# Kernel tuning notes

Measured on AMD Instinct MI355X. Metric: run time of the kernel, lower is better.

The kernel has to match this reference:

```python
import jax, jax.numpy as jnp
import numpy as np

B, S, IN, D, H, L, M = 8, 1024, 256, 512, 8, 2, 64
DK = D // H
FF = 4 * D
EPS = 1e-5


def setup_inputs() -> dict:
    key = jax.random.key(0)
    ks = jax.random.split(key, 16)
    w = lambda k, shape: jax.random.normal(k, shape, jnp.float32) * 0.02
    return {
        "inputs": jax.random.normal(ks[0], (B, S, IN), jnp.float32),
        "lengths": jax.random.randint(ks[1], (B,), S // 2, S + 1),
        "W_in": w(ks[2], (IN, D)), "b_in": jnp.zeros((D,), jnp.float32),
        # per-layer stacked params (leading axis L) for lax.scan
        "Wq": w(ks[3], (L, D, D)), "bq": jnp.zeros((L, D), jnp.float32),
        "Wk": w(ks[4], (L, D, D)), "bk": jnp.zeros((L, D), jnp.float32),
        "Wv": w(ks[5], (L, D, D)), "bv": jnp.zeros((L, D), jnp.float32),
        "Wo": w(ks[6], (L, D, D)), "bo": jnp.zeros((L, D), jnp.float32),
        "rel_bias": w(ks[7], (L, H, 2 * M - 1)),
        "W1": w(ks[8], (L, D, FF)), "b1": jnp.zeros((L, FF), jnp.float32),
        "W2": w(ks[9], (L, FF, D)), "b2": jnp.zeros((L, D), jnp.float32),
        "g1": jnp.ones((L, D), jnp.float32), "be1": jnp.zeros((L, D), jnp.float32),
        "g2": jnp.ones((L, D), jnp.float32), "be2": jnp.zeros((L, D), jnp.float32),
        "gf": jnp.ones((D,), jnp.float32), "bef": jnp.zeros((D,), jnp.float32),
    }


def _ln(x, g, b):
    m = jnp.mean(x, axis=-1, keepdims=True)
    v = jnp.mean(jnp.square(x - m), axis=-1, keepdims=True)
    return (x - m) * jax.lax.rsqrt(v + EPS) * g + b


def _sinusoid_pe(seq_len, d_model):
    pos = jnp.arange(seq_len, dtype=jnp.float32)[:, None]
    div = jnp.exp(jnp.arange(0, d_model, 2, dtype=jnp.float32) * (-np.log(10000.0) / d_model))
    pe = jnp.zeros((seq_len, d_model), jnp.float32)
    pe = pe.at[:, 0::2].set(jnp.sin(pos * div))
    pe = pe.at[:, 1::2].set(jnp.cos(pos * div))
    return pe


def _encoder(inputs, lengths, W_in, b_in, Wq, bq, Wk, bk, Wv, bv, Wo, bo,
             rel_bias, W1, b1, W2, b2, g1, be1, g2, be2, gf, bef):
    x = inputs @ W_in + b_in                      # (B,S,D)
    x = x + _sinusoid_pe(S, D)[None]
    pad = jnp.arange(S)[None, :] >= lengths[:, None]   # (B,S) True = padded key

    r = jnp.arange(S)
    rel_idx = jnp.clip(r[:, None] - r[None, :], -(M - 1), M - 1) + (M - 1)  # (S,S)
    scale = 1.0 / np.sqrt(DK)

    def layer(x, p):
        (wq, bq_, wk, bk_, wv, bv_, wo, bo_, rb, w1, b1_, w2, b2_, g1_, be1_, g2_, be2_) = p
        # --- self-attention sublayer (pre-norm) ---
        h = _ln(x, g1_, be1_)
        q = (h @ wq + bq_).reshape(B, S, H, DK).transpose(0, 2, 1, 3)  # (B,H,S,DK)
        k = (h @ wk + bk_).reshape(B, S, H, DK).transpose(0, 2, 1, 3)
        v = (h @ wv + bv_).reshape(B, S, H, DK).transpose(0, 2, 1, 3)
        scores = jnp.einsum('bhqd,bhkd->bhqk', q, k) * scale
        scores = scores + rb[:, rel_idx][None]            # (H,S,S) relative bias
        scores = jnp.where(pad[:, None, None, :], -jnp.inf, scores)
        attn = jax.nn.softmax(scores, axis=-1)
        o = jnp.einsum('bhqk,bhkd->bhqd', attn, v)
        o = o.transpose(0, 2, 1, 3).reshape(B, S, D) @ wo + bo_
        x = x + o
        # --- FFN sublayer (pre-norm) ---
        h = _ln(x, g2_, be2_)
        x = x + (jax.nn.relu(h @ w1 + b1_) @ w2 + b2_)
        return x, None

    stacked = (Wq, bq, Wk, bk, Wv, bv, Wo, bo, rel_bias, W1, b1, W2, b2, g1, be1, g2, be2)
    x, _ = jax.lax.scan(layer, x, stacked)
    return _ln(x, gf, bef)


def reference(inputs, lengths, W_in, b_in, Wq, bq, Wk, bk, Wv, bv, Wo, bo,
              rel_bias, W1, b1, W2, b2, g1, be1, g2, be2, gf, bef):
    return _encoder(inputs, lengths, W_in, b_in, Wq, bq, Wk, bk, Wv, bv, Wo, bo,
                    rel_bias, W1, b1, W2, b2, g1, be1, g2, be2, gf, bef)
```

## Files before the change

kernel.cpp:

```cpp
#include <hip/hip_runtime.h>
#include <hip/hip_bf16.h>

typedef unsigned short u16;
typedef unsigned int u32;
typedef __bf16 v8bf __attribute__((ext_vector_type(8)));
typedef float v4f __attribute__((ext_vector_type(4)));

#define B_SZ 8
#define S_LEN 1024
#define IN_DIM 256
#define DMODEL 512
#define NHEAD 8
#define DK 64
#define FF_DIM 2048
#define MROWS (B_SZ * S_LEN)
#define QSCALE 0.1803368801111204f

__device__ __forceinline__ u16 f2bf(float f) {
    unsigned int x = __float_as_uint(f);
    unsigned int r = (x + 0x7fffu + ((x >> 16) & 1u)) >> 16;
    return (u16)r;
}

__device__ __forceinline__ void gl16(const u16* g, u16* l) {
    __builtin_amdgcn_global_load_lds((const __attribute__((address_space(1))) unsigned int*)g,
                                     (__attribute__((address_space(3))) unsigned int*)l, 16, 0, 0);
}

__global__ __launch_bounds__(256) void conv_bf16_kernel(const float* __restrict__ in,
                                                        u16* __restrict__ out, int n4) {
    int i = blockIdx.x * 256 + threadIdx.x;
    if (i < n4) {
        float4 v = ((const float4*)in)[i];
        ushort4 o;
        o.x = f2bf(v.x); o.y = f2bf(v.y); o.z = f2bf(v.z); o.w = f2bf(v.w);
        ((ushort4*)out)[i] = o;
    }
}

struct TDesc { const float* src; u16* dst; int K; int N; };
struct TArgs { TDesc d[13]; };

__global__ void transpose_conv_kernel(TArgs args) {
    TDesc t = args.d[blockIdx.z];
    int k0 = blockIdx.x * 32, n0 = blockIdx.y * 32;
    if (k0 >= t.K || n0 >= t.N) return;
    __shared__ float tile[32][33];
    int tx = threadIdx.x, ty = threadIdx.y;
#pragma unroll
    for (int j = 0; j < 4; j++) {
        int k = k0 + ty + j * 8;
        tile[ty + j * 8][tx] = t.src[(size_t)k * t.N + n0 + tx];
    }
    __syncthreads();
#pragma unroll
    for (int j = 0; j < 4; j++) {
        int n = n0 + ty + j * 8;
        t.dst[(size_t)n * t.K + k0 + tx] = f2bf(tile[tx][ty + j * 8]);
    }
}

template <bool OUT_BF16>
__global__ __launch_bounds__(256) void ln_kernel(const float* __restrict__ x,
                                                 const float* __restrict__ g,
                                                 const float* __restrict__ b,
                                                 void* __restrict__ out) {
    int row = blockIdx.x * 4 + (threadIdx.x >> 6);
    int lane = threadIdx.x & 63;
    const float4* xr = (const float4*)(x + (size_t)row * DMODEL);
    float4 v0 = xr[lane], v1 = xr[lane + 64];
    float s = v0.x + v0.y + v0.z + v0.w + v1.x + v1.y + v1.z + v1.w;
    float sq = v0.x * v0.x + v0.y * v0.y + v0.z * v0.z + v0.w * v0.w +
               v1.x * v1.x + v1.y * v1.y + v1.z * v1.z + v1.w * v1.w;
#pragma unroll
    for (int m = 1; m < 64; m <<= 1) {
        s += __shfl_xor(s, m);
        sq += __shfl_xor(sq, m);
    }
    float mean = s * (1.0f / DMODEL);
    float var = sq * (1.0f / DMODEL) - mean * mean;
    float rstd = rsqrtf(var + 1e-5f);
    const float4* g4 = (const float4*)g;
    const float4* b4 = (const float4*)b;
    float4 ga = g4[lane], gb = g4[lane + 64], ba = b4[lane], bb = b4[lane + 64];
    float4 r0, r1;
    r0.x = (v0.x - mean) * rstd * ga.x + ba.x;
    r0.y = (v0.y - mean) * rstd * ga.y + ba.y;
    r0.z = (v0.z - mean) * rstd * ga.z + ba.z;
    r0.w = (v0.w - mean) * rstd * ga.w + ba.w;
    r1.x = (v1.x - mean) * rstd * gb.x + bb.x;
    r1.y = (v1.y - mean) * rstd * gb.y + bb.y;
    r1.z = (v1.z - mean) * rstd * gb.z + bb.z;
    r1.w = (v1.w - mean) * rstd * gb.w + bb.w;
    if (OUT_BF16) {
        ushort4 o0, o1;
        o0.x = f2bf(r0.x); o0.y = f2bf(r0.y); o0.z = f2bf(r0.z); o0.w = f2bf(r0.w);
        o1.x = f2bf(r1.x); o1.y = f2bf(r1.y); o1.z = f2bf(r1.z); o1.w = f2bf(r1.w);
        ((ushort4*)out)[(size_t)row * 128 + lane] = o0;
        ((ushort4*)out)[(size_t)row * 128 + 64 + lane] = o1;
    } else {
        ((float4*)out)[(size_t)row * 128 + lane] = r0;
        ((float4*)out)[(size_t)row * 128 + 64 + lane] = r1;
    }
}

template <int MT, int NT>
__device__ __forceinline__ void gemm_core(const u16* __restrict__ A, const u16* __restrict__ Bt,
                                          int K, v4f (&acc)[MT][NT]) {
    constexpr int BM = MT * 32;
    constexpr int BN = NT * 32;
    __shared__ u16 As[BM * 64];
    __shared__ u16 Bs[BN * 64];
    int tid = threadIdx.x;
    int n0 = blockIdx.x * BN, m0 = blockIdx.y * BM;
    int w = tid >> 6, lane = tid & 63;
    int wr = (w >> 1) * (BM / 2), wc = (w & 1) * (BN / 2);
    int lr = lane & 15, lq = lane >> 4;
    int r8 = lane >> 3, cb = lane & 7;
    int scol = (cb ^ r8) * 8;

    v4f zero = {0.f, 0.f, 0.f, 0.f};
#pragma unroll
    for (int i = 0; i < MT; i++)
#pragma unroll
        for (int j = 0; j < NT; j++) acc[i][j] = zero;

    const u16* gA[MT]; u16* lA[MT];
#pragma unroll
    for (int j = 0; j < MT; j++) {
        int row0 = (MT * 8) * w + j * 8;
        gA[j] = A + (size_t)(m0 + row0 + r8) * K + scol;
        lA[j] = As + row0 * 64;
    }
    const u16* gB[NT]; u16* lB[NT];
#pragma unroll
    for (int j = 0; j < NT; j++) {
        int row0 = (NT * 8) * w + j * 8;
        gB[j] = Bt + (size_t)(n0 + row0 + r8) * K + scol;
        lB[j] = Bs + row0 * 64;
    }

    for (int k0 = 0; k0 < K; k0 += 64) {
#pragma unroll
        for (int j = 0; j < MT; j++) gl16(gA[j], lA[j]);
#pragma unroll
        for (int j = 0; j < NT; j++) gl16(gB[j], lB[j]);
        __syncthreads();
#pragma unroll
        for (int kk = 0; kk < 2; kk++) {
            int xb = ((kk * 4 + lq) ^ (lr & 7)) * 8;
            v8bf af[MT], bfr[NT];
#pragma unroll
            for (int i = 0; i < MT; i++)
                af[i] = *(const v8bf*)&As[(wr + i * 16 + lr) * 64 + xb];
#pragma unroll
            for (int j = 0; j < NT; j++)
                bfr[j] = *(const v8bf*)&Bs[(wc + j * 16 + lr) * 64 + xb];
#pragma unroll
            for (int mt = 0; mt < MT; mt++)
#pragma unroll
                for (int nt = 0; nt < NT; nt++)
                    acc[mt][nt] = __builtin_amdgcn_mfma_f32_16x16x32_bf16(af[mt], bfr[nt], acc[mt][nt], 0, 0, 0);
        }
        __syncthreads();
#pragma unroll
        for (int j = 0; j < MT; j++) gA[j] += 64;
#pragma unroll
        for (int j = 0; j < NT; j++) gB[j] += 64;
    }
}

__global__ __launch_bounds__(256) void gemm_in_kernel(const u16* __restrict__ A,
                                                      const u16* __restrict__ Bt,
                                                      const float* __restrict__ bias,
                                                      float* __restrict__ Out, int K) {
    v4f acc[4][2];
    gemm_core<4, 2>(A, Bt, K, acc);
    int tid = threadIdx.x, w = tid >> 6, lane = tid & 63;
    int lr = lane & 15, lq = lane >> 4;
    int wr = (w >> 1) * 64, wc = (w & 1) * 32;
    int n0 = blockIdx.x * 64, m0 = blockIdx.y * 128;
#pragma unroll
    for (int mt = 0; mt < 4; mt++) {
#pragma unroll
        for (int nt = 0; nt < 2; nt++) {
            int col = n0 + wc + nt * 16 + lr;
            float bcol = bias[col];
            float freq = __builtin_amdgcn_exp2f((float)(col & ~1) * (-0.025953277f));
#pragma unroll
            for (int reg = 0; reg < 4; reg++) {
                int row = m0 + wr + mt * 16 + lq * 4 + reg;
                float rev = (float)(row & (S_LEN - 1)) * freq * 0.15915494309189535f;
                float fr = __builtin_amdgcn_fractf(rev);
                float pe = (col & 1) ? __builtin_amdgcn_cosf(fr) : __builtin_amdgcn_sinf(fr);
                Out[(size_t)row * DMODEL + col] = acc[mt][nt][reg] + bcol + pe;
            }
        }
    }
}

__global__ __launch_bounds__(256) void gemm_qkv_kernel(const u16* __restrict__ A,
                                                       const u16* __restrict__ Bt,
                                                       const float* __restrict__ bq,
                                                       const float* __restrict__ bk,
                                                       const float* __restrict__ bv,
                                                       u16* __restrict__ Qo,
                                                       u16* __restrict__ Ko,
                                                       u16* __restrict__ Vto, int K) {
    v4f acc[4][4];
    gemm_core<4, 4>(A, Bt, K, acc);
    int tid = threadIdx.x, w = tid >> 6, lane = tid & 63;
    int lr = lane & 15, lq = lane >> 4;
    int wr = (w >> 1) * 64, wc = (w & 1) * 64;
    int n0 = blockIdx.x * 128, m0 = blockIdx.y * 128;
    int seg = n0 >> 9;
#pragma unroll
    for (int mt = 0; mt < 4; mt++) {
#pragma unroll
        for (int nt = 0; nt < 4; nt++) {
            int col = (n0 + wc + nt * 16 + lr) & (DMODEL - 1);
            if (seg == 0) {
                float bcol = bq[col];
#pragma unroll
                for (int reg = 0; reg < 4; reg++) {
                    int row = m0 + wr + mt * 16 + lq * 4 + reg;
                    Qo[(size_t)row * DMODEL + col] = f2bf((acc[mt][nt][reg] + bcol) * QSCALE);
                }
            } else if (seg == 1) {
                float bcol = bk[col];
#pragma unroll
                for (int reg = 0; reg < 4; reg++) {
                    int row = m0 + wr + mt * 16 + lq * 4 + reg;
                    Ko[(size_t)row * DMODEL + col] = f2bf(acc[mt][nt][reg] + bcol);
                }
            } else {
                float bcol = bv[col];
                int row0 = m0 + wr + mt * 16 + lq * 4;
                int bb = row0 >> 10, s0 = row0 & (S_LEN - 1);
                ushort4 o;
                o.x = f2bf(acc[mt][nt][0] + bcol);
                o.y = f2bf(acc[mt][nt][1] + bcol);
                o.z = f2bf(acc[mt][nt][2] + bcol);
                o.w = f2bf(acc[mt][nt][3] + bcol);
                *(ushort4*)(Vto + ((size_t)(bb * DMODEL + col)) * S_LEN + s0) = o;
            }
        }
    }
}

__global__ __launch_bounds__(256) void gemm_relu_kernel(const u16* __restrict__ A,
                                                        const u16* __restrict__ Bt,
                                                        const float* __restrict__ bias,
                                                        u16* __restrict__ Out, int N, int K) {
    v4f acc[4][4];
    gemm_core<4, 4>(A, Bt, K, acc);
    int tid = threadIdx.x, w = tid >> 6, lane = tid & 63;
    int lr = lane & 15, lq = lane >> 4;
    int wr = (w >> 1) * 64, wc = (w & 1) * 64;
    int n0 = blockIdx.x * 128, m0 = blockIdx.y * 128;
#pragma unroll
    for (int mt = 0; mt < 4; mt++) {
#pragma unroll
        for (int nt = 0; nt < 4; nt++) {
            int col = n0 + wc + nt * 16 + lr;
            float bcol = bias[col];
#pragma unroll
            for (int reg = 0; reg < 4; reg++) {
                int row = m0 + wr + mt * 16 + lq * 4 + reg;
                Out[(size_t)row * N + col] = f2bf(fmaxf(acc[mt][nt][reg] + bcol, 0.0f));
            }
        }
    }
}

__global__ __launch_bounds__(256) void gemm_res_kernel(const u16* __restrict__ A,
                                                       const u16* __restrict__ Bt,
                                                       const float* __restrict__ bias,
                                                       float* __restrict__ Out, int K) {
    v4f acc[4][2];
    gemm_core<4, 2>(A, Bt, K, acc);
    int tid = threadIdx.x, w = tid >> 6, lane = tid & 63;
    int lr = lane & 15, lq = lane >> 4;
    int wr = (w >> 1) * 64, wc = (w & 1) * 32;
    int n0 = blockIdx.x * 64, m0 = blockIdx.y * 128;
#pragma unroll
    for (int mt = 0; mt < 4; mt++) {
#pragma unroll
        for (int nt = 0; nt < 2; nt++) {
            int col = n0 + wc + nt * 16 + lr;
            float bcol = bias[col];
#pragma unroll
            for (int reg = 0; reg < 4; reg++) {
                int row = m0 + wr + mt * 16 + lq * 4 + reg;
                size_t idx = (size_t)row * DMODEL + col;
                Out[idx] = Out[idx] + acc[mt][nt][reg] + bcol;
            }
        }
    }
}

#define LDP 68
__global__ __launch_bounds__(256) void fattn_kernel(const u16* __restrict__ Qg,
                                                    const u16* __restrict__ Kg,
                                                    const u16* __restrict__ Vtg,
                                                    const float* __restrict__ rb,
                                                    const int* __restrict__ lengths,
                                                    u16* __restrict__ O) {
    int qt = blockIdx.x, h = blockIdx.y, b = blockIdx.z;
    int tid = threadIdx.x, w = tid >> 6, lane = tid & 63;
    int lr = lane & 15, lq = lane >> 4;
    __shared__ u16 Ks[2][64 * 64];
    __shared__ u16 Vs[2][64 * 64];
    __shared__ u16 Pw[4][32 * LDP];
    __shared__ float rbs[128];
    int len = lengths[b];
    if (tid < 127) rbs[tid] = rb[h * 127 + tid] * 1.4426950408889634f;

    int qw = qt * 128 + w * 32;
    v8bf qa[2][2];
#pragma unroll
    for (int ntq = 0; ntq < 2; ntq++) {
        size_t qrow = ((size_t)(b * S_LEN + qw + ntq * 16 + lr)) * DMODEL + h * DK;
        qa[ntq][0] = *(const v8bf*)(Qg + qrow + lq * 8);
        qa[ntq][1] = *(const v8bf*)(Qg + qrow + 32 + lq * 8);
    }

    v4f zero = {0.f, 0.f, 0.f, 0.f};
    v4f Oacc[2][4];
#pragma unroll
    for (int mt = 0; mt < 2; mt++)
#pragma unroll
        for (int nt = 0; nt < 4; nt++) Oacc[mt][nt] = zero;
    float lsum[2] = {0.f, 0.f};

    const u16* Kbase = Kg + ((size_t)b * S_LEN) * DMODEL + h * DK;
    const u16* Vbase = Vtg + ((size_t)(b * DMODEL + h * DK)) * S_LEN;
    u16* P = Pw[w];
    int r8 = lane >> 3, cb = lane & 7;
    int swz = (cb ^ r8) * 8;

#pragma unroll
    for (int j = 0; j < 2; j++) {
        int row0 = w * 16 + j * 8;
        gl16(Kbase + (size_t)(row0 + r8) * DMODEL + swz, Ks[0] + row0 * 64);
        gl16(Vbase + (size_t)(row0 + r8) * S_LEN + swz, Vs[0] + row0 * 64);
    }

    int pb = 0;
    for (int kb0 = 0; kb0 < len; kb0 += 64, pb ^= 1) {
        __syncthreads();
        __builtin_amdgcn_sched_barrier(0);

        int nxt = kb0 + 64;
        if (nxt < len) {
#pragma unroll
            for (int j = 0; j < 2; j++) {
                int row0 = w * 16 + j * 8;
                gl16(Kbase + (size_t)(nxt + row0 + r8) * DMODEL + swz, Ks[pb ^ 1] + row0 * 64);
                gl16(Vbase + (size_t)(row0 + r8) * S_LEN + nxt + swz, Vs[pb ^ 1] + row0 * 64);
            }
        }
        const u16* Ksc = Ks[pb];
        const u16* Vsc = Vs[pb];

        v8bf kf[4][2];
#pragma unroll
        for (int mtk = 0; mtk < 4; mtk++) {
#pragma unroll
            for (int half = 0; half < 2; half++) {
                int xb = ((half * 4 + lq) ^ (lr & 7)) * 8;
                kf[mtk][half] = *(const v8bf*)&Ksc[(mtk * 16 + lr) * 64 + xb];
            }
        }

        v4f S[4][2];
#pragma unroll
        for (int mtk = 0; mtk < 4; mtk++)
#pragma unroll
            for (int ntq = 0; ntq < 2; ntq++) {
                v4f s = __builtin_amdgcn_mfma_f32_16x16x32_bf16(kf[mtk][0], qa[ntq][0], zero, 0, 0, 0);
                S[mtk][ntq] = __builtin_amdgcn_mfma_f32_16x16x32_bf16(kf[mtk][1], qa[ntq][1], s, 0, 0, 0);
            }

        bool edge = (kb0 + 64 > len);
        int dmin = qw - (kb0 + 63), dmax = qw + 31 - kb0;
        bool perel = !(dmax <= -63 || dmin >= 63);
        float bconst = (dmax <= -63) ? rbs[0] : rbs[126];
#pragma unroll
        for (int mtk = 0; mtk < 4; mtk++) {
#pragma unroll
            for (int ntq = 0; ntq < 2; ntq++) {
                int q = qw + ntq * 16 + lr;
                float p[4];
#pragma unroll
                for (int r = 0; r < 4; r++) {
                    int key = kb0 + mtk * 16 + lq * 4 + r;
                    float s = S[mtk][ntq][r];
                    if (perel) {
                        int d = q - key;
                        d = d < -63 ? -63 : (d > 63 ? 63 : d);
                        s += rbs[d + 63];
                    } else {
                        s += bconst;
                    }
                    float pv = __builtin_amdgcn_exp2f(s);
                    if (edge && key >= len) pv = 0.f;
                    lsum[ntq] += pv;
                    p[r] = pv;
                }
                uint2 pk;
                pk.x = (__float_as_uint(p[1]) & 0xffff0000u) | (__float_as_uint(p[0]) >> 16);
                pk.y = (__float_as_uint(p[3]) & 0xffff0000u) | (__float_as_uint(p[2]) >> 16);
                *(uint2*)&P[(ntq * 16 + lr) * LDP + mtk * 16 + lq * 4] = pk;
            }
        }

        v8bf vb[4][2];
#pragma unroll
        for (int ntd = 0; ntd < 4; ntd++) {
#pragma unroll
            for (int half = 0; half < 2; half++) {
                int xb = ((half * 4 + lq) ^ (lr & 7)) * 8;
                vb[ntd][half] = *(const v8bf*)&Vsc[(ntd * 16 + lr) * 64 + xb];
            }
        }
#pragma unroll
        for (int mtq = 0; mtq < 2; mtq++) {
            v8bf pa0 = *(const v8bf*)&P[(mtq * 16 + lr) * LDP + lq * 8];
            v8bf pa1 = *(const v8bf*)&P[(mtq * 16 + lr) * LDP + 32 + lq * 8];
#pragma unroll
            for (int ntd = 0; ntd < 4; ntd++) {
                Oacc[mtq][ntd] = __builtin_amdgcn_mfma_f32_16x16x32_bf16(pa0, vb[ntd][0], Oacc[mtq][ntd], 0, 0, 0);
                Oacc[mtq][ntd] = __builtin_amdgcn_mfma_f32_16x16x32_bf16(pa1, vb[ntd][1], Oacc[mtq][ntd], 0, 0, 0);
            }
        }
    }

    float lsumR[2];
#pragma unroll
    for (int ntq = 0; ntq < 2; ntq++) {
        float s = lsum[ntq];
        s += __shfl_xor(s, 16);
        s += __shfl_xor(s, 32);
        lsumR[ntq] = s;
    }
#pragma unroll
    for (int mtq = 0; mtq < 2; mtq++) {
        float inv[4];
#pragma unroll
        for (int r = 0; r < 4; r++)
            inv[r] = 1.0f / __shfl(lsumR[mtq], lq * 4 + r);
        size_t obase = ((size_t)(b * S_LEN + qw + mtq * 16)) * DMODEL + h * DK;
#pragma unroll
        for (int ntd = 0; ntd < 4; ntd++)
#pragma unroll
            for (int r = 0; r < 4; r++)
                O[obase + (size_t)(lq * 4 + r) * DMODEL + ntd * 16 + lr] = f2bf(Oacc[mtq][ntd][r] * inv[r]);
    }
}

extern "C" void kernel_launch(void* const* d_in, const int* in_sizes, int n_in,
                              void* d_out, int out_size, void* d_ws, size_t ws_size,
                              hipStream_t stream) {
    const float* inputs   = (const float*)d_in[0];
    const int*   lengths  = (const int*)d_in[1];
    const float* W_in     = (const float*)d_in[2];
    const float* b_in     = (const float*)d_in[3];
    const float* Wq       = (const float*)d_in[4];
    const float* bq       = (const float*)d_in[5];
    const float* Wk       = (const float*)d_in[6];
    const float* bk       = (const float*)d_in[7];
    const float* Wv       = (const float*)d_in[8];
    const float* bv       = (const float*)d_in[9];
    const float* Wo       = (const float*)d_in[10];
    const float* bo       = (const float*)d_in[11];
    const float* rel_bias = (const float*)d_in[12];
    const float* W1       = (const float*)d_in[13];
    const float* b1       = (const float*)d_in[14];
    const float* W2       = (const float*)d_in[15];
    const float* b2       = (const float*)d_in[16];
    const float* g1       = (const float*)d_in[17];
    const float* be1      = (const float*)d_in[18];
    const float* g2       = (const float*)d_in[19];
    const float* be2      = (const float*)d_in[20];
    const float* gf       = (const float*)d_in[21];
    const float* bef      = (const float*)d_in[22];

    char* ws = (char*)d_ws;
    float* xbuf = (float*)ws;          ws += (size_t)MROWS * DMODEL * 4;
    u16* hbuf   = (u16*)ws;            ws += (size_t)MROWS * DMODEL * 2;
    u16* aobuf  = hbuf;
    u16* qbf    = (u16*)ws;            ws += (size_t)MROWS * FF_DIM * 2;
    u16* kbf    = qbf + (size_t)MROWS * DMODEL;
    u16* vtbf   = kbf + (size_t)MROWS * DMODEL;
    u16* tbuf   = qbf;
    u16* inbf   = qbf;
    u16* wt_in  = (u16*)ws;            ws += (size_t)DMODEL * IN_DIM * 2;
    u16 *qkvw[2], *wto[2], *wt1[2], *wt2[2];
    for (int l = 0; l < 2; l++) { qkvw[l] = (u16*)ws; ws += (size_t)3 * DMODEL * DMODEL * 2; }
    for (int l = 0; l < 2; l++) { wto[l] = (u16*)ws; ws += (size_t)DMODEL * DMODEL * 2; }
    for (int l = 0; l < 2; l++) { wt1[l] = (u16*)ws; ws += (size_t)FF_DIM * DMODEL * 2; }
    for (int l = 0; l < 2; l++) { wt2[l] = (u16*)ws; ws += (size_t)DMODEL * FF_DIM * 2; }

    TArgs ta;
    int ti = 0;
    ta.d[ti++] = {W_in, wt_in, IN_DIM, DMODEL};
    for (int l = 0; l < 2; l++) {
        ta.d[ti++] = {Wq + (size_t)l * DMODEL * DMODEL, qkvw[l], DMODEL, DMODEL};
        ta.d[ti++] = {Wk + (size_t)l * DMODEL * DMODEL, qkvw[l] + (size_t)DMODEL * DMODEL, DMODEL, DMODEL};
        ta.d[ti++] = {Wv + (size_t)l * DMODEL * DMODEL, qkvw[l] + (size_t)2 * DMODEL * DMODEL, DMODEL, DMODEL};
        ta.d[ti++] = {Wo + (size_t)l * DMODEL * DMODEL, wto[l], DMODEL, DMODEL};
        ta.d[ti++] = {W1 + (size_t)l * DMODEL * FF_DIM, wt1[l], DMODEL, FF_DIM};
        ta.d[ti++] = {W2 + (size_t)l * FF_DIM * DMODEL, wt2[l], FF_DIM, DMODEL};
    }

    conv_bf16_kernel<<<dim3((MROWS * IN_DIM / 4 + 255) / 256), 256, 0, stream>>>(
        inputs, inbf, MROWS * IN_DIM / 4);
    transpose_conv_kernel<<<dim3(64, 64, 13), dim3(32, 8), 0, stream>>>(ta);

    gemm_in_kernel<<<dim3(DMODEL / 64, MROWS / 128), 256, 0, stream>>>(
        inbf, wt_in, b_in, xbuf, IN_DIM);

    for (int l = 0; l < 2; l++) {
        ln_kernel<true><<<MROWS / 4, 256, 0, stream>>>(xbuf, g1 + l * DMODEL, be1 + l * DMODEL, hbuf);
        gemm_qkv_kernel<<<dim3(3 * DMODEL / 128, MROWS / 128), 256, 0, stream>>>(
            hbuf, qkvw[l], bq + l * DMODEL, bk + l * DMODEL, bv + l * DMODEL,
            qbf, kbf, vtbf, DMODEL);
        fattn_kernel<<<dim3(S_LEN / 128, NHEAD, B_SZ), 256, 0, stream>>>(
            qbf, kbf, vtbf, rel_bias + (size_t)l * NHEAD * 127, lengths, aobuf);
        gemm_res_kernel<<<dim3(DMODEL / 64, MROWS / 128), 256, 0, stream>>>(
            aobuf, wto[l], bo + l * DMODEL, xbuf, DMODEL);
        ln_kernel<true><<<MROWS / 4, 256, 0, stream>>>(xbuf, g2 + l * DMODEL, be2 + l * DMODEL, hbuf);
        gemm_relu_kernel<<<dim3(FF_DIM / 128, MROWS / 128), 256, 0, stream>>>(
            hbuf, wt1[l], b1 + l * FF_DIM, tbuf, FF_DIM, DMODEL);
        gemm_res_kernel<<<dim3(DMODEL / 64, MROWS / 128), 256, 0, stream>>>(
            tbuf, wt2[l], b2 + l * DMODEL, xbuf, FF_DIM);
    }
    ln_kernel<false><<<MROWS / 4, 256, 0, stream>>>(xbuf, gf, bef, d_out);
}
```

Before: 469.3 us.

## Halve attention query tile, remap blocks across XCDs, add MFMA priority hints

The flash-attention kernel now gives each wave 16 query rows instead of 32, so a block covers 64 queries and the grid doubles to 1024 one-dimensional blocks. Block IDs are remapped so that consecutive blocks sharing a batch/head land on the same XCD, which should improve L2 reuse of K/V. s_setprio hints are placed around the MFMA sections. The larger grid raises occupancy and parallelism but loads each K/V tile twice as often per query processed, which adds memory traffic.

Result: slower. 496.6 us (+5.8%).

```diff
diff --git a/kernel.cpp b/kernel.cpp
--- a/kernel.cpp
+++ b/kernel.cpp
@@ -306,32 +306,33 @@
                                                     const float* __restrict__ rb,
                                                     const int* __restrict__ lengths,
                                                     u16* __restrict__ O) {
-    int qt = blockIdx.x, h = blockIdx.y, b = blockIdx.z;
+    int bid = blockIdx.x;
+    int wg = (bid & 7) * 128 + (bid >> 3);
+    int qt = wg & 15;
+    int bh = wg >> 4;
+    int h = bh & 7, b = bh >> 3;
     int tid = threadIdx.x, w = tid >> 6, lane = tid & 63;
     int lr = lane & 15, lq = lane >> 4;
     __shared__ u16 Ks[2][64 * 64];
     __shared__ u16 Vs[2][64 * 64];
-    __shared__ u16 Pw[4][32 * LDP];
+    __shared__ u16 Pw[4][16 * LDP];
     __shared__ float rbs[128];
     int len = lengths[b];
     if (tid < 127) rbs[tid] = rb[h * 127 + tid] * 1.4426950408889634f;
 
-    int qw = qt * 128 + w * 32;
-    v8bf qa[2][2];
-#pragma unroll
-    for (int ntq = 0; ntq < 2; ntq++) {
-        size_t qrow = ((size_t)(b * S_LEN + qw + ntq * 16 + lr)) * DMODEL + h * DK;
-        qa[ntq][0] = *(const v8bf*)(Qg + qrow + lq * 8);
-        qa[ntq][1] = *(const v8bf*)(Qg + qrow + 32 + lq * 8);
+    int qw = qt * 64 + w * 16;
+    v8bf qa[2];
+    {
+        size_t qrow = ((size_t)(b * S_LEN + qw + lr)) * DMODEL + h * DK;
+        qa[0] = *(const v8bf*)(Qg + qrow + lq * 8);
+        qa[1] = *(const v8bf*)(Qg + qrow + 32 + lq * 8);
     }
 
     v4f zero = {0.f, 0.f, 0.f, 0.f};
-    v4f Oacc[2][4];
-#pragma unroll
-    for (int mt = 0; mt < 2; mt++)
-#pragma unroll
-        for (int nt = 0; nt < 4; nt++) Oacc[mt][nt] = zero;
-    float lsum[2] = {0.f, 0.f};
+    v4f Oacc[4];
+#pragma unroll
+    for (int nt = 0; nt < 4; nt++) Oacc[nt] = zero;
+    float lsum = 0.f;
 
     const u16* Kbase = Kg + ((size_t)b * S_LEN) * DMODEL + h * DK;
     const u16* Vbase = Vtg + ((size_t)(b * DMODEL + h * DK)) * S_LEN;
@@ -373,46 +374,43 @@
             }
         }
 
-        v4f S[4][2];
-#pragma unroll
-        for (int mtk = 0; mtk < 4; mtk++)
-#pragma unroll
-            for (int ntq = 0; ntq < 2; ntq++) {
-                v4f s = __builtin_amdgcn_mfma_f32_16x16x32_bf16(kf[mtk][0], qa[ntq][0], zero, 0, 0, 0);
-                S[mtk][ntq] = __builtin_amdgcn_mfma_f32_16x16x32_bf16(kf[mtk][1], qa[ntq][1], s, 0, 0, 0);
-            }
+        v4f S[4];
+        __builtin_amdgcn_s_setprio(1);
+#pragma unroll
+        for (int mtk = 0; mtk < 4; mtk++) {
+            v4f s = __builtin_amdgcn_mfma_f32_16x16x32_bf16(kf[mtk][0], qa[0], zero, 0, 0, 0);
+            S[mtk] = __builtin_amdgcn_mfma_f32_16x16x32_bf16(kf[mtk][1], qa[1], s, 0, 0, 0);
+        }
+        __builtin_amdgcn_s_setprio(0);
 
         bool edge = (kb0 + 64 > len);
-        int dmin = qw - (kb0 + 63), dmax = qw + 31 - kb0;
+        int dmin = qw - (kb0 + 63), dmax = qw + 15 - kb0;
         bool perel = !(dmax <= -63 || dmin >= 63);
         float bconst = (dmax <= -63) ? rbs[0] : rbs[126];
+        int q = qw + lr;
 #pragma unroll
         for (int mtk = 0; mtk < 4; mtk++) {
-#pragma unroll
-            for (int ntq = 0; ntq < 2; ntq++) {
-                int q = qw + ntq * 16 + lr;
-                float p[4];
-#pragma unroll
-                for (int r = 0; r < 4; r++) {
-                    int key = kb0 + mtk * 16 + lq * 4 + r;
-                    float s = S[mtk][ntq][r];
-                    if (perel) {
-                        int d = q - key;
-                        d = d < -63 ? -63 : (d > 63 ? 63 : d);
-                        s += rbs[d + 63];
-                    } else {
-                        s += bconst;
-                    }
-                    float pv = __builtin_amdgcn_exp2f(s);
-                    if (edge && key >= len) pv = 0.f;
-                    lsum[ntq] += pv;
-                    p[r] = pv;
+            float p[4];
+#pragma unroll
+            for (int r = 0; r < 4; r++) {
+                int key = kb0 + mtk * 16 + lq * 4 + r;
+                float s = S[mtk][r];
+                if (perel) {
+                    int d = q - key;
+                    d = d < -63 ? -63 : (d > 63 ? 63 : d);
+                    s += rbs[d + 63];
+                } else {
+                    s += bconst;
                 }
-                uint2 pk;
-                pk.x = (__float_as_uint(p[1]) & 0xffff0000u) | (__float_as_uint(p[0]) >> 16);
-                pk.y = (__float_as_uint(p[3]) & 0xffff0000u) | (__float_as_uint(p[2]) >> 16);
-                *(uint2*)&P[(ntq * 16 + lr) * LDP + mtk * 16 + lq * 4] = pk;
-            }
+                float pv = __builtin_amdgcn_exp2f(s);
+                if (edge && key >= len) pv = 0.f;
+                lsum += pv;
+                p[r] = pv;
+            }
+            uint2 pk;
+            pk.x = (__float_as_uint(p[1]) & 0xffff0000u) | (__float_as_uint(p[0]) >> 16);
+            pk.y = (__float_as_uint(p[3]) & 0xffff0000u) | (__float_as_uint(p[2]) >> 16);
+            *(uint2*)&P[lr * LDP + mtk * 16 + lq * 4] = pk;
         }
 
         v8bf vb[4][2];
@@ -424,39 +422,30 @@
                 vb[ntd][half] = *(const v8bf*)&Vsc[(ntd * 16 + lr) * 64 + xb];
             }
         }
-#pragma unroll
-        for (int mtq = 0; mtq < 2; mtq++) {
-            v8bf pa0 = *(const v8bf*)&P[(mtq * 16 + lr) * LDP + lq * 8];
-            v8bf pa1 = *(const v8bf*)&P[(mtq * 16 + lr) * LDP + 32 + lq * 8];
-#pragma unroll
-            for (int ntd = 0; ntd < 4; ntd++) {
-                Oacc[mtq][ntd] = __builtin_amdgcn_mfma_f32_16x16x32_bf16(pa0, vb[ntd][0], Oacc[mtq][ntd], 0, 0, 0);
-                Oacc[mtq][ntd] = __builtin_amdgcn_mfma_f32_16x16x32_bf16(pa1, vb[ntd][1], Oacc[mtq][ntd], 0, 0, 0);
-            }
-        }
-    }
-
-    float lsumR[2];
-#pragma unroll
-    for (int ntq = 0; ntq < 2; ntq++) {
-        float s = lsum[ntq];
-        s += __shfl_xor(s, 16);
-        s += __shfl_xor(s, 32);
-        lsumR[ntq] = s;
-    }
-#pragma unroll
-    for (int mtq = 0; mtq < 2; mtq++) {
-        float inv[4];
+        v8bf pa0 = *(const v8bf*)&P[lr * LDP + lq * 8];
+        v8bf pa1 = *(const v8bf*)&P[lr * LDP + 32 + lq * 8];
+        __builtin_amdgcn_s_setprio(1);
+#pragma unroll
+        for (int ntd = 0; ntd < 4; ntd++) {
+            Oacc[ntd] = __builtin_amdgcn_mfma_f32_16x16x32_bf16(pa0, vb[ntd][0], Oacc[ntd], 0, 0, 0);
+            Oacc[ntd] = __builtin_amdgcn_mfma_f32_16x16x32_bf16(pa1, vb[ntd][1], Oacc[ntd], 0, 0, 0);
+        }
+        __builtin_amdgcn_s_setprio(0);
+    }
+
+    float lsumR = lsum;
+    lsumR += __shfl_xor(lsumR, 16);
+    lsumR += __shfl_xor(lsumR, 32);
+    float inv[4];
+#pragma unroll
+    for (int r = 0; r < 4; r++)
+        inv[r] = 1.0f / __shfl(lsumR, lq * 4 + r);
+    size_t obase = ((size_t)(b * S_LEN + qw)) * DMODEL + h * DK;
+#pragma unroll
+    for (int ntd = 0; ntd < 4; ntd++)
 #pragma unroll
         for (int r = 0; r < 4; r++)
-            inv[r] = 1.0f / __shfl(lsumR[mtq], lq * 4 + r);
-        size_t obase = ((size_t)(b * S_LEN + qw + mtq * 16)) * DMODEL + h * DK;
-#pragma unroll
-        for (int ntd = 0; ntd < 4; ntd++)
-#pragma unroll
-            for (int r = 0; r < 4; r++)
-                O[obase + (size_t)(lq * 4 + r) * DMODEL + ntd * 16 + lr] = f2bf(Oacc[mtq][ntd][r] * inv[r]);
-    }
+            O[obase + (size_t)(lq * 4 + r) * DMODEL + ntd * 16 + lr] = f2bf(Oacc[ntd][r] * inv[r]);
 }
 
 extern "C" void kernel_launch(void* const* d_in, const int* in_sizes, int n_in,
@@ -526,7 +515,7 @@
         gemm_qkv_kernel<<<dim3(3 * DMODEL / 128, MROWS / 128), 256, 0, stream>>>(
             hbuf, qkvw[l], bq + l * DMODEL, bk + l * DMODEL, bv + l * DMODEL,
             qbf, kbf, vtbf, DMODEL);
-        fattn_kernel<<<dim3(S_LEN / 128, NHEAD, B_SZ), 256, 0, stream>>>(
+        fattn_kernel<<<dim3(1024), 256, 0, stream>>>(
             qbf, kbf, vtbf, rel_bias + (size_t)l * NHEAD * 127, lengths, aobuf);
         gemm_res_kernel<<<dim3(DMODEL / 64, MROWS / 128), 256, 0, stream>>>(
             aobuf, wto[l], bo + l * DMODEL, xbuf, DMODEL);
```

## Split attention over key halves with a combine pass and XCD-aware block mapping

Applied to the files above, without the earlier changes.

The flash-attention kernel now splits each (batch, head, query-tile) over two key ranges, so there are twice as many blocks, each writing an unnormalized partial output plus row sums. A new combine kernel adds the two halves and normalizes. This works because softmax here uses no running max, so partials add directly. Block ids are remapped so the halves and tiles interleave across XCDs, and s_setprio brackets the MFMA sections. The cost is an extra kernel launch and more memory traffic: the partials go to the output buffer and the sums to scratch. Rounding the partials to bf16 before combining also adds some precision loss.

New measurement: 495.7 us. +5.6%, slower.

```diff
diff --git a/kernel.cpp b/kernel.cpp
--- a/kernel.cpp
+++ b/kernel.cpp
@@ -305,8 +305,14 @@
                                                     const u16* __restrict__ Vtg,
                                                     const float* __restrict__ rb,
                                                     const int* __restrict__ lengths,
-                                                    u16* __restrict__ O) {
-    int qt = blockIdx.x, h = blockIdx.y, b = blockIdx.z;
+                                                    u16* __restrict__ Op,
+                                                    float* __restrict__ lsums) {
+    int bid = blockIdx.x;
+    int wg = (bid & 7) * 128 + (bid >> 3);
+    int half = wg & 1;
+    int qt = (wg >> 1) & 7;
+    int bh = wg >> 4;
+    int h = bh & 7, b = bh >> 3;
     int tid = threadIdx.x, w = tid >> 6, lane = tid & 63;
     int lr = lane & 15, lq = lane >> 4;
     __shared__ u16 Ks[2][64 * 64];
@@ -316,6 +322,9 @@
     int len = lengths[b];
     if (tid < 127) rbs[tid] = rb[h * 127 + tid] * 1.4426950408889634f;
 
+    int kstart = half * 512;
+    int kend = half ? len : 512;
+
     int qw = qt * 128 + w * 32;
     v8bf qa[2][2];
 #pragma unroll
@@ -342,17 +351,17 @@
 #pragma unroll
     for (int j = 0; j < 2; j++) {
         int row0 = w * 16 + j * 8;
-        gl16(Kbase + (size_t)(row0 + r8) * DMODEL + swz, Ks[0] + row0 * 64);
-        gl16(Vbase + (size_t)(row0 + r8) * S_LEN + swz, Vs[0] + row0 * 64);
+        gl16(Kbase + (size_t)(kstart + row0 + r8) * DMODEL + swz, Ks[0] + row0 * 64);
+        gl16(Vbase + (size_t)(row0 + r8) * S_LEN + kstart + swz, Vs[0] + row0 * 64);
     }
 
     int pb = 0;
-    for (int kb0 = 0; kb0 < len; kb0 += 64, pb ^= 1) {
+    for (int kb0 = kstart; kb0 < kend; kb0 += 64, pb ^= 1) {
         __syncthreads();
         __builtin_amdgcn_sched_barrier(0);
 
         int nxt = kb0 + 64;
-        if (nxt < len) {
+        if (nxt < kend) {
 #pragma unroll
             for (int j = 0; j < 2; j++) {
                 int row0 = w * 16 + j * 8;
@@ -367,13 +376,14 @@
 #pragma unroll
         for (int mtk = 0; mtk < 4; mtk++) {
 #pragma unroll
-            for (int half = 0; half < 2; half++) {
-                int xb = ((half * 4 + lq) ^ (lr & 7)) * 8;
-                kf[mtk][half] = *(const v8bf*)&Ksc[(mtk * 16 + lr) * 64 + xb];
+            for (int half_ = 0; half_ < 2; half_++) {
+                int xb = ((half_ * 4 + lq) ^ (lr & 7)) * 8;
+                kf[mtk][half_] = *(const v8bf*)&Ksc[(mtk * 16 + lr) * 64 + xb];
             }
         }
 
         v4f S[4][2];
+        __builtin_amdgcn_s_setprio(1);
 #pragma unroll
         for (int mtk = 0; mtk < 4; mtk++)
 #pragma unroll
@@ -381,6 +391,7 @@
                 v4f s = __builtin_amdgcn_mfma_f32_16x16x32_bf16(kf[mtk][0], qa[ntq][0], zero, 0, 0, 0);
                 S[mtk][ntq] = __builtin_amdgcn_mfma_f32_16x16x32_bf16(kf[mtk][1], qa[ntq][1], s, 0, 0, 0);
             }
+        __builtin_amdgcn_s_setprio(0);
 
         bool edge = (kb0 + 64 > len);
         int dmin = qw - (kb0 + 63), dmax = qw + 31 - kb0;
@@ -419,11 +430,12 @@
 #pragma unroll
         for (int ntd = 0; ntd < 4; ntd++) {
 #pragma unroll
-            for (int half = 0; half < 2; half++) {
-                int xb = ((half * 4 + lq) ^ (lr & 7)) * 8;
-                vb[ntd][half] = *(const v8bf*)&Vsc[(ntd * 16 + lr) * 64 + xb];
-            }
-        }
+            for (int half_ = 0; half_ < 2; half_++) {
+                int xb = ((half_ * 4 + lq) ^ (lr & 7)) * 8;
+                vb[ntd][half_] = *(const v8bf*)&Vsc[(ntd * 16 + lr) * 64 + xb];
+            }
+        }
+        __builtin_amdgcn_s_setprio(1);
 #pragma unroll
         for (int mtq = 0; mtq < 2; mtq++) {
             v8bf pa0 = *(const v8bf*)&P[(mtq * 16 + lr) * LDP + lq * 8];
@@ -434,6 +446,7 @@
                 Oacc[mtq][ntd] = __builtin_amdgcn_mfma_f32_16x16x32_bf16(pa1, vb[ntd][1], Oacc[mtq][ntd], 0, 0, 0);
             }
         }
+        __builtin_amdgcn_s_setprio(0);
     }
 
     float lsumR[2];
@@ -444,19 +457,49 @@
         s += __shfl_xor(s, 32);
         lsumR[ntq] = s;
     }
+    if (lq == 0) {
+#pragma unroll
+        for (int ntq = 0; ntq < 2; ntq++) {
+            int q = qw + ntq * 16 + lr;
+            lsums[((size_t)half * MROWS + b * S_LEN + q) * NHEAD + h] = lsumR[ntq];
+        }
+    }
+    u16* Oh = Op + (size_t)half * MROWS * DMODEL;
 #pragma unroll
     for (int mtq = 0; mtq < 2; mtq++) {
-        float inv[4];
-#pragma unroll
-        for (int r = 0; r < 4; r++)
-            inv[r] = 1.0f / __shfl(lsumR[mtq], lq * 4 + r);
         size_t obase = ((size_t)(b * S_LEN + qw + mtq * 16)) * DMODEL + h * DK;
 #pragma unroll
         for (int ntd = 0; ntd < 4; ntd++)
 #pragma unroll
             for (int r = 0; r < 4; r++)
-                O[obase + (size_t)(lq * 4 + r) * DMODEL + ntd * 16 + lr] = f2bf(Oacc[mtq][ntd][r] * inv[r]);
-    }
+                Oh[obase + (size_t)(lq * 4 + r) * DMODEL + ntd * 16 + lr] = f2bf(Oacc[mtq][ntd][r]);
+    }
+}
+
+__device__ __forceinline__ u32 comb2(u32 a, u32 b, float inv) {
+    float r0 = (__uint_as_float(a << 16) + __uint_as_float(b << 16)) * inv;
+    float r1 = (__uint_as_float(a & 0xffff0000u) + __uint_as_float(b & 0xffff0000u)) * inv;
+    return (u32)f2bf(r0) | ((u32)f2bf(r1) << 16);
+}
+
+__global__ __launch_bounds__(256) void attn_combine_kernel(const u16* __restrict__ Op,
+                                                           const float* __restrict__ lsums,
+                                                           u16* __restrict__ out) {
+    int row = blockIdx.x * 4 + (threadIdx.x >> 6);
+    int lane = threadIdx.x & 63;
+    int h = lane >> 3;
+    float l0 = lsums[(size_t)row * NHEAD + h];
+    float l1 = lsums[((size_t)MROWS + row) * NHEAD + h];
+    float inv = 1.0f / (l0 + l1);
+    size_t base = (size_t)row * DMODEL + lane * 8;
+    uint4 a = *(const uint4*)(Op + base);
+    uint4 c = *(const uint4*)(Op + (size_t)MROWS * DMODEL + base);
+    uint4 o;
+    o.x = comb2(a.x, c.x, inv);
+    o.y = comb2(a.y, c.y, inv);
+    o.z = comb2(a.z, c.z, inv);
+    o.w = comb2(a.w, c.w, inv);
+    *(uint4*)(out + base) = o;
 }
 
 extern "C" void kernel_launch(void* const* d_in, const int* in_sizes, int n_in,
@@ -493,8 +536,10 @@
     u16* qbf    = (u16*)ws;            ws += (size_t)MROWS * FF_DIM * 2;
     u16* kbf    = qbf + (size_t)MROWS * DMODEL;
     u16* vtbf   = kbf + (size_t)MROWS * DMODEL;
+    float* lsums = (float*)(vtbf + (size_t)MROWS * DMODEL);
     u16* tbuf   = qbf;
     u16* inbf   = qbf;
+    u16* opart  = (u16*)d_out;
     u16* wt_in  = (u16*)ws;            ws += (size_t)DMODEL * IN_DIM * 2;
     u16 *qkvw[2], *wto[2], *wt1[2], *wt2[2];
     for (int l = 0; l < 2; l++) { qkvw[l] = (u16*)ws; ws += (size_t)3 * DMODEL * DMODEL * 2; }
@@ -526,8 +571,9 @@
         gemm_qkv_kernel<<<dim3(3 * DMODEL / 128, MROWS / 128), 256, 0, stream>>>(
             hbuf, qkvw[l], bq + l * DMODEL, bk + l * DMODEL, bv + l * DMODEL,
             qbf, kbf, vtbf, DMODEL);
-        fattn_kernel<<<dim3(S_LEN / 128, NHEAD, B_SZ), 256, 0, stream>>>(
-            qbf, kbf, vtbf, rel_bias + (size_t)l * NHEAD * 127, lengths, aobuf);
+        fattn_kernel<<<dim3(1024), 256, 0, stream>>>(
+            qbf, kbf, vtbf, rel_bias + (size_t)l * NHEAD * 127, lengths, opart, lsums);
+        attn_combine_kernel<<<MROWS / 4, 256, 0, stream>>>(opart, lsums, aobuf);
         gemm_res_kernel<<<dim3(DMODEL / 64, MROWS / 128), 256, 0, stream>>>(
             aobuf, wto[l], bo + l * DMODEL, xbuf, DMODEL);
         ln_kernel<true><<<MROWS / 4, 256, 0, stream>>>(xbuf, g2 + l * DMODEL, be2 + l * DMODEL, hbuf);
```
